# Optimization experiments

Measured on AMD Instinct MI355X. Metric: run time of the kernel, lower is better.

Reference implementation:

```python
import jax, jax.numpy as jnp
import numpy as np


def setup_inputs() -> dict:
    key = jax.random.key(0)
    x = jax.random.normal(key, (8, 192, 64, 64), dtype=jnp.float32)
    return {"x": x}


def reference(x):
    # x: [b, c, h, w]
    b, c, h, w = x.shape
    xf = x.reshape(b, c, h * w)                                   # [b, c, hw]
    # prepend global-mean token -> [b, c, T] with T = hw + 1
    xf = jnp.concatenate([xf.mean(axis=-1, keepdims=True), xf], axis=-1)
    scale = jnp.asarray(c, xf.dtype) ** -0.25                      # 1/sqrt(sqrt(c))
    qs = xf * scale
    # full T x T score matrix, as in the original module
    weight = jnp.einsum('bct,bcs->bts', qs, qs)                    # [b, T, T]
    weight = jax.nn.softmax(weight.astype(jnp.float32), axis=-1).astype(xf.dtype)
    out = jnp.einsum('bts,bcs->bct', weight, xf)                   # [b, c, T]
    return out[:, :, 0]                                            # [b, c]
```

## Files before the change

kernel.cpp:

```cpp
#include <hip/hip_runtime.h>

#define BB 8
#define CC 192
#define HWN 4096
#define SCALE2 0.07216878364870323f
#define NCHUNK 128
#define CW 32


#define GLOAD_LDS16(gp, lp)                                                    \
    __builtin_amdgcn_global_load_lds(                                          \
        (const __attribute__((address_space(1))) void*)(gp),                   \
        (__attribute__((address_space(3))) void*)(lp), 16, 0, 0)

__global__ void mean_kernel(const float* __restrict__ x, float* __restrict__ m) {
    int wave = threadIdx.x >> 6, lane = threadIdx.x & 63;
    int bc = blockIdx.x * 4 + wave;
    const float4* p4 = (const float4*)(x + (size_t)bc * HWN);
    float s = 0.f;
#pragma unroll
    for (int i = 0; i < 16; ++i) {
        float4 v = p4[lane + 64 * i];
        s += v.x + v.y + v.z + v.w;
    }
    for (int off = 32; off; off >>= 1) s += __shfl_down(s, off);
    if (lane == 0) m[bc] = s * (1.0f / HWN);
}

__global__ __launch_bounds__(256)
void fused_kernel(const float* __restrict__ x,
                  const float* __restrict__ m,
                  float* __restrict__ Zp,
                  float* __restrict__ Op) {
    const int chunk = blockIdx.x;
    const int b     = blockIdx.y;
    const int t     = threadIdx.x;

    __shared__ float tile[CC * CW];
    __shared__ float ml[CC];
    __shared__ float scp[256];
    __shared__ float wls[CW];

    const float* xb = x + (size_t)b * CC * HWN + chunk * CW;
#pragma unroll
    for (int it = 0; it < 6; ++it) {
        int i = t + it * 256;
        int c = i >> 3, k = i & 7;
        const float* gsrc = xb + (size_t)c * HWN + 4 * k;
        float* ldst = tile + 4 * (i & ~63);
        GLOAD_LDS16(gsrc, ldst);
    }
    if (t < CC) ml[t] = m[b * CC + t];
    __syncthreads();

    {
        int g = t >> 5, s = t & 31;
        int c0 = g * 24;
        float acc = 0.f;
#pragma unroll
        for (int c = 0; c < 24; ++c)
            acc += ml[c0 + c] * tile[(c0 + c) * CW + s];
        scp[t] = acc;
    }
    __syncthreads();

    if (t < CW) {
        float sc = 0.f;
#pragma unroll
        for (int g = 0; g < 8; ++g) sc += scp[g * 32 + t];
        float w = __expf(sc * SCALE2);
        wls[t] = w;
        float se = w;
        for (int off = 16; off; off >>= 1) se += __shfl_xor(se, off);
        if (t == 0) Zp[b * NCHUNK + chunk] = se;
    }
    __syncthreads();

    if (t < CC) {
        const float4* t4 = (const float4*)(tile + t * CW);
        const float4* w4 = (const float4*)wls;
        float o = 0.f;
#pragma unroll
        for (int j = 0; j < 8; ++j) {
            int sg = (t + j) & 7;
            float4 v = t4[sg];
            float4 w = w4[sg];
            o += v.x * w.x + v.y * w.y + v.z * w.z + v.w * w.w;
        }
        Op[((size_t)b * NCHUNK + chunk) * CC + t] = o;
    }
}

__global__ __launch_bounds__(512)
void combine_kernel(const float* __restrict__ m,
                    const float* __restrict__ Zp,
                    const float* __restrict__ Op,
                    float* __restrict__ out) {
    int cg = blockIdx.x;
    int b  = blockIdx.y;
    int t  = threadIdx.x;
    __shared__ float psum[512];
    __shared__ float sInv, sE0;

    if (t < 64) {
        float z = Zp[b * NCHUNK + t] + Zp[b * NCHUNK + 64 + t];
        float q = m[b * CC + t] * m[b * CC + t]
                + m[b * CC + 64 + t] * m[b * CC + 64 + t]
                + m[b * CC + 128 + t] * m[b * CC + 128 + t];
        for (int off = 32; off; off >>= 1) {
            z += __shfl_xor(z, off);
            q += __shfl_xor(q, off);
        }
        if (t == 0) {
            float e0 = __expf(q * SCALE2);
            sE0 = e0;
            sInv = 1.0f / (z + e0);
        }
    }

    int grp = t >> 6;
    int c   = cg * 64 + (t & 63);
    const float* op = Op + ((size_t)b * NCHUNK + grp * 16) * CC + c;
    float acc = 0.f;
#pragma unroll
    for (int j = 0; j < 16; ++j)
        acc += op[(size_t)j * CC];
    psum[t] = acc;
    __syncthreads();

    if (t < 64) {
        float o = 0.f;
#pragma unroll
        for (int g = 0; g < 8; ++g)
            o += psum[g * 64 + t];
        int cc = cg * 64 + t;
        out[b * CC + cc] = (o + sE0 * m[b * CC + cc]) * sInv;
    }
}

extern "C" void kernel_launch(void* const* d_in, const int* in_sizes, int n_in,
                              void* d_out, int out_size, void* d_ws, size_t ws_size,
                              hipStream_t stream) {
    const float* x = (const float*)d_in[0];
    float* out = (float*)d_out;

    float* ws = (float*)d_ws;
    float* m  = ws;
    float* Zp = ws + 1536;
    float* Op = ws + 2560;

    mean_kernel<<<BB * CC / 4, 256, 0, stream>>>(x, m);
    fused_kernel<<<dim3(NCHUNK, BB), 256, 0, stream>>>(x, m, Zp, Op);
    combine_kernel<<<dim3(3, BB), 512, 0, stream>>>(m, Zp, Op, out);
}
```

Before: 17.76 us.

## Split mean reduction into halves, vectorize score partials, widen combine block

The mean kernel now has two waves per channel, each summing half the spatial extent and writing raw partial sums, so twice as many blocks are launched. Downstream kernels add the two halves and scale by 1/HW on the fly. The fused kernel's score partial products now use float4 tile reads with 32 channel groups instead of 8, which shortens each thread's serial loop but lengthens the final 32-term reduction done by one wave. The combine kernel moves to 1024 threads, each summing 8 chunk partials instead of 16.

```diff
diff --git a/kernel.cpp b/kernel.cpp
--- a/kernel.cpp
+++ b/kernel.cpp
@@ -4,6 +4,7 @@
 #define CC 192
 #define HWN 4096
 #define SCALE2 0.07216878364870323f
+#define INVHW (1.0f / HWN)
 #define NCHUNK 128
 #define CW 32
 
@@ -13,33 +14,35 @@
         (const __attribute__((address_space(1))) void*)(gp),                   \
         (__attribute__((address_space(3))) void*)(lp), 16, 0, 0)
 
-__global__ void mean_kernel(const float* __restrict__ x, float* __restrict__ m) {
-    int wave = threadIdx.x >> 6, lane = threadIdx.x & 63;
-    int bc = blockIdx.x * 4 + wave;
-    const float4* p4 = (const float4*)(x + (size_t)bc * HWN);
+__global__ __launch_bounds__(256)
+void mean_kernel(const float* __restrict__ x, float* __restrict__ mh) {
+    int w = threadIdx.x >> 6, lane = threadIdx.x & 63;
+    int ch   = blockIdx.x * 2 + (w >> 1);
+    int half = w & 1;
+    const float4* p4 = (const float4*)(x + (size_t)ch * HWN + half * (HWN / 2));
     float s = 0.f;
 #pragma unroll
-    for (int i = 0; i < 16; ++i) {
-        float4 v = p4[lane + 64 * i];
+    for (int k = 0; k < 8; ++k) {
+        float4 v = p4[lane + 64 * k];
         s += v.x + v.y + v.z + v.w;
     }
     for (int off = 32; off; off >>= 1) s += __shfl_down(s, off);
-    if (lane == 0) m[bc] = s * (1.0f / HWN);
+    if (lane == 0) mh[half * 1536 + ch] = s;
 }
 
 __global__ __launch_bounds__(256)
 void fused_kernel(const float* __restrict__ x,
-                  const float* __restrict__ m,
+                  const float* __restrict__ mh,
                   float* __restrict__ Zp,
                   float* __restrict__ Op) {
     const int chunk = blockIdx.x;
     const int b     = blockIdx.y;
     const int t     = threadIdx.x;
 
-    __shared__ float tile[CC * CW];
-    __shared__ float ml[CC];
-    __shared__ float scp[256];
-    __shared__ float wls[CW];
+    __shared__ float  tile[CC * CW];
+    __shared__ float  ml[CC];
+    __shared__ float4 scp4[256];
+    __shared__ float  wls[CW];
 
     const float* xb = x + (size_t)b * CC * HWN + chunk * CW;
 #pragma unroll
@@ -50,24 +53,30 @@
         float* ldst = tile + 4 * (i & ~63);
         GLOAD_LDS16(gsrc, ldst);
     }
-    if (t < CC) ml[t] = m[b * CC + t];
+    if (t < CC) ml[t] = (mh[b * CC + t] + mh[1536 + b * CC + t]) * INVHW;
     __syncthreads();
 
     {
-        int g = t >> 5, s = t & 31;
-        int c0 = g * 24;
-        float acc = 0.f;
+        int g = t >> 3, sq = t & 7;
+        const float4* t4 = (const float4*)tile;
+        float4 a = make_float4(0.f, 0.f, 0.f, 0.f);
 #pragma unroll
-        for (int c = 0; c < 24; ++c)
-            acc += ml[c0 + c] * tile[(c0 + c) * CW + s];
-        scp[t] = acc;
+        for (int c = 0; c < 6; ++c) {
+            int r = g * 6 + c;
+            float4 v = t4[r * 8 + sq];
+            float mlv = ml[r];
+            a.x += mlv * v.x; a.y += mlv * v.y;
+            a.z += mlv * v.z; a.w += mlv * v.w;
+        }
+        scp4[t] = a;
     }
     __syncthreads();
 
+    const float* scp = (const float*)scp4;
     if (t < CW) {
         float sc = 0.f;
 #pragma unroll
-        for (int g = 0; g < 8; ++g) sc += scp[g * 32 + t];
+        for (int g = 0; g < 32; ++g) sc += scp[g * 32 + t];
         float w = __expf(sc * SCALE2);
         wls[t] = w;
         float se = w;
@@ -91,22 +100,26 @@
     }
 }
 
-__global__ __launch_bounds__(512)
-void combine_kernel(const float* __restrict__ m,
+__global__ __launch_bounds__(1024)
+void combine_kernel(const float* __restrict__ mh,
                     const float* __restrict__ Zp,
                     const float* __restrict__ Op,
                     float* __restrict__ out) {
     int cg = blockIdx.x;
     int b  = blockIdx.y;
     int t  = threadIdx.x;
-    __shared__ float psum[512];
+    __shared__ float psum[1024];
     __shared__ float sInv, sE0;
 
     if (t < 64) {
         float z = Zp[b * NCHUNK + t] + Zp[b * NCHUNK + 64 + t];
-        float q = m[b * CC + t] * m[b * CC + t]
-                + m[b * CC + 64 + t] * m[b * CC + 64 + t]
-                + m[b * CC + 128 + t] * m[b * CC + 128 + t];
+        float q = 0.f;
+#pragma unroll
+        for (int p = 0; p < 3; ++p) {
+            int i = b * CC + p * 64 + t;
+            float mv = (mh[i] + mh[1536 + i]) * INVHW;
+            q += mv * mv;
+        }
         for (int off = 32; off; off >>= 1) {
             z += __shfl_xor(z, off);
             q += __shfl_xor(q, off);
@@ -120,10 +133,10 @@
 
     int grp = t >> 6;
     int c   = cg * 64 + (t & 63);
-    const float* op = Op + ((size_t)b * NCHUNK + grp * 16) * CC + c;
+    const float* op = Op + ((size_t)b * NCHUNK + grp * 8) * CC + c;
     float acc = 0.f;
 #pragma unroll
-    for (int j = 0; j < 16; ++j)
+    for (int j = 0; j < 8; ++j)
         acc += op[(size_t)j * CC];
     psum[t] = acc;
     __syncthreads();
@@ -131,10 +144,11 @@
     if (t < 64) {
         float o = 0.f;
 #pragma unroll
-        for (int g = 0; g < 8; ++g)
+        for (int g = 0; g < 16; ++g)
             o += psum[g * 64 + t];
-        int cc = cg * 64 + t;
-        out[b * CC + cc] = (o + sE0 * m[b * CC + cc]) * sInv;
+        int i = b * CC + cg * 64 + t;
+        float mv = (mh[i] + mh[1536 + i]) * INVHW;
+        out[i] = (o + sE0 * mv) * sInv;
     }
 }
 
@@ -145,11 +159,11 @@
     float* out = (float*)d_out;
 
     float* ws = (float*)d_ws;
-    float* m  = ws;
-    float* Zp = ws + 1536;
-    float* Op = ws + 2560;
+    float* mh = ws;
+    float* Zp = ws + 3072;
+    float* Op = ws + 4096;
 
-    mean_kernel<<<BB * CC / 4, 256, 0, stream>>>(x, m);
-    fused_kernel<<<dim3(NCHUNK, BB), 256, 0, stream>>>(x, m, Zp, Op);
-    combine_kernel<<<dim3(3, BB), 512, 0, stream>>>(m, Zp, Op, out);
+    mean_kernel<<<BB * CC / 2, 256, 0, stream>>>(x, mh);
+    fused_kernel<<<dim3(NCHUNK, BB), 256, 0, stream>>>(x, mh, Zp, Op);
+    combine_kernel<<<dim3(3, BB), 1024, 0, stream>>>(mh, Zp, Op, out);
 }
```

Result: slower. 18.45 us (+3.9%).
